# Optimization experiments

Hardware: AMD Instinct MI355X
Metric: run time of the kernel (lower is better)

## Reference

```python
import jax, jax.numpy as jnp
import numpy as np
import math

B, L, T, IN, H, DEPTH, HEADS = 4096, 1, 64, 16, 128, 3, 2
HD = H // HEADS
EPS = 1e-5


def layer_norm(x, g, b):
    u = jnp.mean(x, axis=-1, keepdims=True)
    s = jnp.mean((x - u) ** 2, axis=-1, keepdims=True)
    return g * (x - u) / jnp.sqrt(s + EPS) + b


def mlp(x, W, b, g, beta):
    return jax.nn.relu(layer_norm(x @ W + b, g, beta))


def attention(h, amask, Wq, bq, Wk, bk, Wv, bv):
    N, Tn, _ = h.shape
    def heads(x):
        return x.reshape(N, Tn, HEADS, HD).transpose(0, 2, 1, 3)
    q = heads(h @ Wq + bq)
    k = heads(h @ Wk + bk)
    v = heads(h @ Wv + bv)
    scores = jnp.einsum('nhqd,nhkd->nhqk', q, k) / math.sqrt(HD)
    scores = scores + (1.0 - amask[:, None]) * -10000.0
    probs = jax.nn.softmax(scores, axis=-1)
    ctx = jnp.einsum('nhqk,nhkd->nhqd', probs, v)
    return ctx.transpose(0, 2, 1, 3).reshape(N, Tn, H)


def setup_inputs() -> dict:
    key = jax.random.key(0)
    ks = jax.random.split(key, 8)
    feat = jax.random.normal(ks[0], (B, L, T, IN), jnp.float32)
    seq_lens = jax.random.randint(ks[1], (B, L), 1, T + 1)
    pos = jnp.arange(T)
    # repo convention: 0 = valid node, 1 = padded; prefix-valid layout
    masks = (pos[None, None, :] >= seq_lens[..., None]).astype(jnp.float32)[..., None]
    s = 0.02
    W_emb = jax.random.normal(ks[2], (IN, H), jnp.float32) * s
    W_enc = jax.random.normal(ks[3], (H, H), jnp.float32) * s
    Wq = jax.random.normal(ks[4], (DEPTH, H, H), jnp.float32) * s
    Wk = jax.random.normal(ks[5], (DEPTH, H, H), jnp.float32) * s
    Wv = jax.random.normal(ks[6], (DEPTH, H, H), jnp.float32) * s
    return dict(
        lane_nodes_feat=feat, masks=masks,
        W_emb=W_emb, b_emb=jnp.zeros((H,)), g_emb=jnp.ones((H,)), beta_emb=jnp.zeros((H,)),
        W_enc=W_enc, b_enc=jnp.zeros((H,)), g_enc=jnp.ones((H,)), beta_enc=jnp.zeros((H,)),
        Wq=Wq, bq=jnp.zeros((DEPTH, H)), Wk=Wk, bk=jnp.zeros((DEPTH, H)), Wv=Wv, bv=jnp.zeros((DEPTH, H)),
        ln_g=jnp.ones((DEPTH, H)), ln_b=jnp.zeros((DEPTH, H)),
    )


def reference(lane_nodes_feat, masks, W_emb, b_emb, g_emb, beta_emb, W_enc, b_enc,
              g_enc, beta_enc, Wq, bq, Wk, bk, Wv, bv, ln_g, ln_b):
    emb = mlp(lane_nodes_feat, W_emb, b_emb, g_emb, beta_emb)   # [B,L,T,H]
    emb = mlp(emb, W_enc, b_enc, g_enc, beta_enc)
    # every (b,l) lane has >=1 valid node by construction, so masked_select == reshape
    hs = emb.reshape(B * L, T, H)
    seq_lens = jnp.sum(1.0 - masks[:, :, :, 0], axis=-1).reshape(B * L)  # [N]
    pos = jnp.arange(T)
    valid = pos[None, :] < seq_lens[:, None]                              # [N,T]
    amask = (valid[:, :, None] & valid[:, None, :]).astype(hs.dtype)      # [N,T,T]
    for d in range(DEPTH):
        temp = hs
        hs = attention(hs, amask, Wq[d], bq[d], Wk[d], bk[d], Wv[d], bv[d])
        hs = jax.nn.relu(hs) + temp
        hs = layer_norm(hs, ln_g[d], ln_b[d])
    hs = jnp.max(hs, axis=1)                                              # [N,H]
    return hs.reshape(B, L, H)
```

## Files before the change

### kernel.cpp

```cpp
#include <hip/hip_runtime.h>

typedef unsigned short u16;
typedef unsigned int u32;
typedef __attribute__((ext_vector_type(8))) short short8;
typedef __attribute__((ext_vector_type(4))) float floatx4;

#define EPSV 1e-5f
#define WS_ELEMS 167936

__device__ __forceinline__ float b2f(u16 u){
  union { float f; u32 i; } c; c.i = ((u32)u) << 16; return c.f;
}
__device__ __forceinline__ u16 f2b(float f){
  union { float f; u32 i; } c; c.f = f;
  u32 r = c.i + 0x7FFFu + ((c.i >> 16) & 1u);
  return (u16)(r >> 16);
}
__device__ __forceinline__ u16 f2bc(float f){
  union { float f; u32 i; } c; c.f = f;
  return (u16)((c.i + 0x8000u) >> 16);
}
__device__ __forceinline__ float ldf(const void* p, int i, bool isf){
  return isf ? ((const float*)p)[i] : b2f(((const u16*)p)[i]);
}
__device__ __forceinline__ bool detect_f32(const void* g_emb){
  return *(const u32*)g_emb == 0x3F800000u;
}
__device__ __forceinline__ void dma16(const u16* g, u16* l){
  __builtin_amdgcn_global_load_lds((const __attribute__((address_space(1))) u32*)(g),
                                   (__attribute__((address_space(3))) u32*)(l), 16, 0, 0);
}
__device__ __forceinline__ void dma_slab(const u16* g, u16* dst, int wave, int lane){
  #pragma unroll
  for (int i = 0; i < 4; i++){
    int c = (wave << 2) + i;
    dma16(g + (c << 9) + (lane << 3), dst + (c << 9));
  }
}

__global__ void prep_kernel(const void* W_emb, const void* W_enc,
                            const void* Wq, const void* Wk, const void* Wv,
                            const void* g_emb, u16* ws){
  bool isf = detect_f32(g_emb);
  int e = blockIdx.x * 256 + threadIdx.x;
  if (e >= WS_ELEMS) return;
  float v;
  if (e < 4096){
    int half = e >> 11, r = e & 2047;
    int nt = r >> 9, q = (r >> 3) & 63, j = r & 7;
    int col = half*64 + nt*16 + (q & 15);
    int k = (q >> 4)*8 + j;
    v = (k < 16) ? ldf(W_emb, k*128 + col, isf) : 0.0f;
  } else if (e < 20480){
    int i = e - 4096;
    int half = i >> 13, r = i & 8191;
    int chunk = r >> 9, q = (r >> 3) & 63, j = r & 7;
    int ks = chunk >> 2, nt = chunk & 3;
    int col = half*64 + nt*16 + (q & 15);
    int k = ks*32 + (q >> 4)*8 + j;
    v = ldf(W_enc, k*128 + col, isf);
  } else {
    int i = e - 20480;
    int slab = i >> 13, r = i & 8191;
    int dh = slab / 3, which = slab - dh*3;
    int d = dh >> 1, h = dh & 1;
    int chunk = r >> 9, q = (r >> 3) & 63, j = r & 7;
    int ks = chunk >> 2, nt = chunk & 3;
    int col = h*64 + nt*16 + (q & 15);
    int k = ks*32 + (q >> 4)*8 + j;
    const void* W = (which == 0) ? Wv : (which == 1) ? Wk : Wq;
    v = ldf(W, d*16384 + k*128 + col, isf);
  }
  ws[e] = f2b(v);
}

__device__ __forceinline__ short8 frg(const u16* p, int chunk, int lane){
  return *(const short8*)(p + (chunk << 9) + (lane << 3));
}
__device__ __forceinline__ int wfoff(int wave, int nt, int lq, int lc){
  return ((((nt >> 1) << 2) + wave) << 9)
       + ((((((nt << 1) + (lc >> 3)) & 3) << 4) + (lq << 2)) << 3) + (lc & 7);
}
__device__ __forceinline__ int qfoff(int wave, int nt, int lq, int lc){
  return (wave << 10) + ((nt >> 1) << 9)
       + ((((((nt << 1) + (lc >> 3)) & 3) << 4) + (lq << 2)) << 3) + (lc & 7);
}

__device__ __forceinline__ void gemmW(const u16* sh, const u16* slab, int wave, int lane, floatx4* acc){
  #pragma unroll
  for (int ks = 0; ks < 4; ks++){
    short8 a = frg(sh, ks*4 + wave, lane);
    #pragma unroll
    for (int nt = 0; nt < 4; nt++)
      acc[nt] = __builtin_amdgcn_mfma_f32_16x16x32_bf16(a, frg(slab, ks*4 + nt, lane), acc[nt], 0, 0, 0);
  }
}
__device__ __forceinline__ void gemmWT(const u16* sh, const u16* slab, int wave, int lane, floatx4* acc){
  #pragma unroll
  for (int ks = 0; ks < 4; ks++){
    short8 a = frg(slab, ks*4 + wave, lane);
    #pragma unroll
    for (int nt = 0; nt < 4; nt++)
      acc[nt] = __builtin_amdgcn_mfma_f32_16x16x32_bf16(a, frg(sh, ks*4 + nt, lane), acc[nt], 0, 0, 0);
  }
}
__device__ __forceinline__ void gemm64(const u16* areg, const u16* b, int wave, int lane, floatx4* acc){
  #pragma unroll
  for (int ks = 0; ks < 2; ks++){
    short8 a = *(const short8*)(areg + (wave << 10) + (ks << 9) + (lane << 3));
    #pragma unroll
    for (int nt = 0; nt < 4; nt++)
      acc[nt] = __builtin_amdgcn_mfma_f32_16x16x32_bf16(a, frg(b, ks*4 + nt, lane), acc[nt], 0, 0, 0);
  }
}

__device__ __forceinline__ void red_sum2(float* s1, float* s2){
  #pragma unroll
  for (int m = 1; m < 16; m <<= 1){
    #pragma unroll
    for (int r = 0; r < 4; r++){
      s1[r] += __shfl_xor(s1[r], m, 64);
      s2[r] += __shfl_xor(s2[r], m, 64);
    }
  }
}

__device__ __forceinline__ void ln_mlp(floatx4* acc, const void* bias, const void* g,
    const void* bet, bool isf, float xres[8][4], int wave, int lq, int lc, u16* sh){
  float x[8][4], s1[4] = {0,0,0,0}, s2[4] = {0,0,0,0};
  #pragma unroll
  for (int nt = 0; nt < 8; nt++){
    float bb = ldf(bias, nt*16 + lc, isf);
    #pragma unroll
    for (int r = 0; r < 4; r++){
      float v = acc[nt][r] + bb;
      x[nt][r] = v; s1[r] += v; s2[r] += v*v;
    }
  }
  red_sum2(s1, s2);
  float mean[4], rstd[4];
  #pragma unroll
  for (int r = 0; r < 4; r++){
    mean[r] = s1[r] * (1.0f/128.0f);
    rstd[r] = rsqrtf(s2[r]*(1.0f/128.0f) - mean[r]*mean[r] + EPSV);
  }
  #pragma unroll
  for (int nt = 0; nt < 8; nt++){
    float gg = ldf(g, nt*16 + lc, isf), bb = ldf(bet, nt*16 + lc, isf);
    int o = wfoff(wave, nt, lq, lc);
    #pragma unroll
    for (int r = 0; r < 4; r++){
      float y = fmaxf((x[nt][r] - mean[r]) * rstd[r] * gg + bb, 0.0f);
      xres[nt][r] = y;
      sh[o + 8*r] = f2bc(y);
    }
  }
}

__device__ __forceinline__ void ln_attn(floatx4* ctx, float xres[8][4], const u16* cb,
                                        int wave, int lq, int lc, u16* sh){
  float x[8][4], s1[4] = {0,0,0,0}, s2[4] = {0,0,0,0};
  #pragma unroll
  for (int nt = 0; nt < 8; nt++){
    #pragma unroll
    for (int r = 0; r < 4; r++){
      float v = fmaxf(ctx[nt][r], 0.0f) + xres[nt][r];
      x[nt][r] = v; s1[r] += v; s2[r] += v*v;
    }
  }
  red_sum2(s1, s2);
  float mean[4], rstd[4];
  #pragma unroll
  for (int r = 0; r < 4; r++){
    mean[r] = s1[r] * (1.0f/128.0f);
    rstd[r] = rsqrtf(s2[r]*(1.0f/128.0f) - mean[r]*mean[r] + EPSV);
  }
  #pragma unroll
  for (int nt = 0; nt < 8; nt++){
    float gg = b2f(cb[384 + nt*16 + lc]), bb = b2f(cb[512 + nt*16 + lc]);
    int o = wfoff(wave, nt, lq, lc);
    #pragma unroll
    for (int r = 0; r < 4; r++){
      float y = (x[nt][r] - mean[r]) * rstd[r] * gg + bb;
      xres[nt][r] = y;
      sh[o + 8*r] = f2bc(y);
    }
  }
}

__global__ __launch_bounds__(256, 3)
void fused_kernel(const void* feat, const void* masks,
                  const void* b_emb, const void* g_emb, const void* be_emb,
                  const void* b_enc, const void* g_enc, const void* be_enc,
                  const void* bq, const void* bk, const void* bv,
                  const void* ln_g, const void* ln_b,
                  const u16* ws, void* out){
  __shared__ __align__(16) u16 s_h[8192];
  __shared__ __align__(16) u16 s_w[8192];
  __shared__ __align__(16) u16 s_k[4096];
  __shared__ __align__(16) u16 s_v[4096];
  __shared__ u16 s_c[1920];
  __shared__ float s_valid[64];

  int tid = threadIdx.x;
  int wave = tid >> 6, lane = tid & 63, lq = lane >> 4, lc = lane & 15;
  int n = blockIdx.x;
  bool isf = detect_f32(g_emb);
  const floatx4 z4 = {0.0f, 0.0f, 0.0f, 0.0f};

  dma16(ws + ((wave*2 + 0) << 9) + (lane << 3), s_w + ((wave*2 + 0) << 9));
  dma16(ws + ((wave*2 + 1) << 9) + (lane << 3), s_w + ((wave*2 + 1) << 9));

  if (!isf){
    const u16* fp = (const u16*)feat + n*1024;
    if (tid < 128){
      int t = tid >> 1, half = tid & 1;
      uint4 v = *(const uint4*)(fp + t*16 + half*8);
      *(uint4*)(s_h + ((t >> 4) << 9) + (((half << 4) + (t & 15)) << 3)) = v;
    } else {
      int t = (tid - 128) >> 1, half = 2 + ((tid - 128) & 1);
      uint4 z; z.x = 0; z.y = 0; z.z = 0; z.w = 0;
      *(uint4*)(s_h + ((t >> 4) << 9) + (((half << 4) + (t & 15)) << 3)) = z;
    }
  } else {
    for (int i = tid; i < 2048; i += 256){
      int t = i >> 5, k = i & 31;
      float v = (k < 16) ? ((const float*)feat)[n*1024 + t*16 + k] : 0.0f;
      s_h[((t >> 4) << 9) + ((((k >> 3) << 4) + (t & 15)) << 3) + (k & 7)] = f2b(v);
    }
  }
  for (int i = tid; i < 1920; i += 256){
    int blk = i >> 7, off = i & 127;
    int d = blk / 5, wh = blk - d*5;
    const void* src = (wh == 0) ? bq : (wh == 1) ? bk : (wh == 2) ? bv : (wh == 3) ? ln_g : ln_b;
    s_c[i] = isf ? f2b(((const float*)src)[d*128 + off]) : ((const u16*)src)[d*128 + off];
  }
  if (tid < 64) s_valid[tid] = (ldf(masks, n*64 + tid, isf) == 0.0f) ? 1.0f : 0.0f;
  __syncthreads();

  float xres[8][4];
  floatx4 acc[8];
  #pragma unroll
  for (int i = 0; i < 8; i++) acc[i] = z4;
  {
    short8 a = frg(s_h, wave, lane);
    #pragma unroll
    for (int nt = 0; nt < 4; nt++){
      acc[nt]     = __builtin_amdgcn_mfma_f32_16x16x32_bf16(a, frg(s_w, nt,     lane), acc[nt],     0,0,0);
      acc[4 + nt] = __builtin_amdgcn_mfma_f32_16x16x32_bf16(a, frg(s_w, 4 + nt, lane), acc[4 + nt], 0,0,0);
    }
  }
  __syncthreads();
  dma_slab(ws + 4096, s_w, wave, lane);
  ln_mlp(acc, b_emb, g_emb, be_emb, isf, xres, wave, lq, lc, s_h);
  __syncthreads();

  #pragma unroll
  for (int i = 0; i < 8; i++) acc[i] = z4;
  gemmW(s_h, s_w, wave, lane, acc);
  __syncthreads();
  dma_slab(ws + 12288, s_w, wave, lane);
  __syncthreads();
  gemmW(s_h, s_w, wave, lane, acc + 4);
  __syncthreads();
  dma_slab(ws + 20480, s_w, wave, lane);
  ln_mlp(acc, b_enc, g_enc, be_enc, isf, xres, wave, lq, lc, s_h);
  __syncthreads();

  int sb = 20480;
  for (int d = 0; d < 3; d++){
    const u16* cb = s_c + d*640;
    floatx4 ctx[8];
    #pragma unroll
    for (int i = 0; i < 8; i++) ctx[i] = z4;

    for (int h = 0; h < 2; h++){
      floatx4 pa[4];
      #pragma unroll
      for (int i = 0; i < 4; i++) pa[i] = z4;
      gemmWT(s_h, s_w, wave, lane, pa);
      __syncthreads();
      dma_slab(ws + sb + 8192, s_w, wave, lane);
      {
        float bb4[4];
        #pragma unroll
        for (int r = 0; r < 4; r++) bb4[r] = b2f(cb[256 + h*64 + wave*16 + (lq << 2) + r]);
        #pragma unroll
        for (int nt = 0; nt < 4; nt++){
          int o = wfoff(wave, nt, lq, lc);
          #pragma unroll
          for (int r = 0; r < 4; r++) s_v[o + 8*r] = f2bc(pa[nt][r] + bb4[r]);
        }
      }
      __syncthreads();
      #pragma unroll
      for (int i = 0; i < 4; i++) pa[i] = z4;
      gemmW(s_h, s_w, wave, lane, pa);
      __syncthreads();
      dma_slab(ws + sb + 16384, s_w, wave, lane);
      {
        #pragma unroll
        for (int nt = 0; nt < 4; nt++){
          float bb = b2f(cb[128 + h*64 + nt*16 + lc]);
          int o = wfoff(wave, nt, lq, lc);
          #pragma unroll
          for (int r = 0; r < 4; r++) s_k[o + 8*r] = f2bc(pa[nt][r] + bb);
        }
      }
      __syncthreads();
      #pragma unroll
      for (int i = 0; i < 4; i++) pa[i] = z4;
      gemmW(s_h, s_w, wave, lane, pa);
      __syncthreads();
      {
        #pragma unroll
        for (int nt = 0; nt < 4; nt++){
          float bb = b2f(cb[h*64 + nt*16 + lc]);
          int o = qfoff(wave, nt, lq, lc);
          #pragma unroll
          for (int r = 0; r < 4; r++) s_w[o + 8*r] = f2bc(pa[nt][r] + bb);
        }
      }
      #pragma unroll
      for (int i = 0; i < 4; i++) pa[i] = z4;
      gemm64(s_w, s_k, wave, lane, pa);

      float rv[4], cv[4];
      #pragma unroll
      for (int r = 0; r < 4; r++) rv[r] = s_valid[wave*16 + (lq << 2) + r];
      #pragma unroll
      for (int nt = 0; nt < 4; nt++) cv[nt] = s_valid[nt*16 + lc];

      float p[4][4];
      #pragma unroll
      for (int nt = 0; nt < 4; nt++)
        #pragma unroll
        for (int r = 0; r < 4; r++)
          p[nt][r] = pa[nt][r]*0.125f - 10000.0f*(1.0f - rv[r]*cv[nt]);

      float mx[4];
      #pragma unroll
      for (int r = 0; r < 4; r++)
        mx[r] = fmaxf(fmaxf(p[0][r], p[1][r]), fmaxf(p[2][r], p[3][r]));
      #pragma unroll
      for (int m = 1; m < 16; m <<= 1)
        #pragma unroll
        for (int r = 0; r < 4; r++) mx[r] = fmaxf(mx[r], __shfl_xor(mx[r], m, 64));

      float sm[4] = {0,0,0,0};
      #pragma unroll
      for (int nt = 0; nt < 4; nt++)
        #pragma unroll
        for (int r = 0; r < 4; r++){ p[nt][r] = __expf(p[nt][r] - mx[r]); sm[r] += p[nt][r]; }
      #pragma unroll
      for (int m = 1; m < 16; m <<= 1)
        #pragma unroll
        for (int r = 0; r < 4; r++) sm[r] += __shfl_xor(sm[r], m, 64);

      float inv[4];
      #pragma unroll
      for (int r = 0; r < 4; r++) inv[r] = 1.0f / sm[r];

      #pragma unroll
      for (int nt = 0; nt < 4; nt++){
        int o = qfoff(wave, nt, lq, lc);
        #pragma unroll
        for (int r = 0; r < 4; r++) s_w[o + 8*r] = f2bc(p[nt][r] * inv[r]);
      }
      gemm64(s_w, s_v, wave, lane, ctx + h*4);
      __syncthreads();
      sb += 24576;
      if (!(d == 2 && h == 1)) dma_slab(ws + sb, s_w, wave, lane);
      if (h == 1) ln_attn(ctx, xres, cb, wave, lq, lc, s_h);
      __syncthreads();
    }
  }

  if (tid < 128){
    int col = tid;
    float mxv = -1e30f;
    #pragma unroll 4
    for (int t = 0; t < 64; t++)
      mxv = fmaxf(mxv, b2f(s_h[((((col >> 5) << 2) + (t >> 4)) << 9)
                               + (((((col >> 3) & 3) << 4) + (t & 15)) << 3) + (col & 7)]));
    if (isf) ((float*)out)[n*128 + col] = mxv;
    else     ((u16*)out)[n*128 + col] = f2b(mxv);
  }
}

extern "C" void kernel_launch(void* const* d_in, const int* in_sizes, int n_in,
                              void* d_out, int out_size, void* d_ws, size_t ws_size,
                              hipStream_t stream){
  const void* feat   = d_in[0];
  const void* masks  = d_in[1];
  const void* W_emb  = d_in[2];
  const void* b_emb  = d_in[3];
  const void* g_emb  = d_in[4];
  const void* be_emb = d_in[5];
  const void* W_enc  = d_in[6];
  const void* b_enc  = d_in[7];
  const void* g_enc  = d_in[8];
  const void* be_enc = d_in[9];
  const void* Wq     = d_in[10];
  const void* bq     = d_in[11];
  const void* Wk     = d_in[12];
  const void* bk     = d_in[13];
  const void* Wv     = d_in[14];
  const void* bv     = d_in[15];
  const void* ln_g   = d_in[16];
  const void* ln_b   = d_in[17];
  u16* ws = (u16*)d_ws;

  hipLaunchKernelGGL(prep_kernel, dim3((WS_ELEMS + 255)/256), dim3(256), 0, stream,
                     W_emb, W_enc, Wq, Wk, Wv, g_emb, ws);
  hipLaunchKernelGGL(fused_kernel, dim3(4096), dim3(256), 0, stream,
                     feat, masks, b_emb, g_emb, be_emb, b_enc, g_enc, be_enc,
                     bq, bk, bv, ln_g, ln_b, ws, d_out);
}
```

Measured before the change: 383.1 us.

## Process two sequences per block to reuse weight slabs across both

Each block now handles two sequences, keeping two hidden-state tiles in shared memory and running every weight GEMM on both, so each staged weight slab (and its DMA and barriers) is amortised over twice the work. The grid is halved and launch bounds drop from 3 to 2 blocks per CU, because register use (two sets of accumulators and residuals) and LDS use both grow. The attention core is factored into a helper and run once per sequence, with the second sequence's Q/K/V results held in registers until the first finishes. The risk is lower occupancy and more register pressure, possibly spilling.

Measured after the change: 444.8 us. +16.1%, slower.

```diff
diff --git a/kernel.cpp b/kernel.cpp
--- a/kernel.cpp
+++ b/kernel.cpp
@@ -86,22 +86,32 @@
        + ((((((nt << 1) + (lc >> 3)) & 3) << 4) + (lq << 2)) << 3) + (lc & 7);
 }
 
-__device__ __forceinline__ void gemmW(const u16* sh, const u16* slab, int wave, int lane, floatx4* acc){
+#define MFMA(a,b,c) __builtin_amdgcn_mfma_f32_16x16x32_bf16((a),(b),(c),0,0,0)
+
+__device__ __forceinline__ void gemmW2(const u16* sh0, const u16* sh1, const u16* slab,
+                                       int wave, int lane, floatx4* a0v, floatx4* a1v){
   #pragma unroll
   for (int ks = 0; ks < 4; ks++){
-    short8 a = frg(sh, ks*4 + wave, lane);
-    #pragma unroll
-    for (int nt = 0; nt < 4; nt++)
-      acc[nt] = __builtin_amdgcn_mfma_f32_16x16x32_bf16(a, frg(slab, ks*4 + nt, lane), acc[nt], 0, 0, 0);
-  }
-}
-__device__ __forceinline__ void gemmWT(const u16* sh, const u16* slab, int wave, int lane, floatx4* acc){
+    short8 a0 = frg(sh0, ks*4 + wave, lane);
+    short8 a1 = frg(sh1, ks*4 + wave, lane);
+    #pragma unroll
+    for (int nt = 0; nt < 4; nt++){
+      short8 b = frg(slab, ks*4 + nt, lane);
+      a0v[nt] = MFMA(a0, b, a0v[nt]);
+      a1v[nt] = MFMA(a1, b, a1v[nt]);
+    }
+  }
+}
+__device__ __forceinline__ void gemmWT2(const u16* sh0, const u16* sh1, const u16* slab,
+                                        int wave, int lane, floatx4* a0v, floatx4* a1v){
   #pragma unroll
   for (int ks = 0; ks < 4; ks++){
     short8 a = frg(slab, ks*4 + wave, lane);
     #pragma unroll
-    for (int nt = 0; nt < 4; nt++)
-      acc[nt] = __builtin_amdgcn_mfma_f32_16x16x32_bf16(a, frg(sh, ks*4 + nt, lane), acc[nt], 0, 0, 0);
+    for (int nt = 0; nt < 4; nt++){
+      a0v[nt] = MFMA(a, frg(sh0, ks*4 + nt, lane), a0v[nt]);
+      a1v[nt] = MFMA(a, frg(sh1, ks*4 + nt, lane), a1v[nt]);
+    }
   }
 }
 __device__ __forceinline__ void gemm64(const u16* areg, const u16* b, int wave, int lane, floatx4* acc){
@@ -110,7 +120,7 @@
     short8 a = *(const short8*)(areg + (wave << 10) + (ks << 9) + (lane << 3));
     #pragma unroll
     for (int nt = 0; nt < 4; nt++)
-      acc[nt] = __builtin_amdgcn_mfma_f32_16x16x32_bf16(a, frg(b, ks*4 + nt, lane), acc[nt], 0, 0, 0);
+      acc[nt] = MFMA(a, frg(b, ks*4 + nt, lane), acc[nt]);
   }
 }
 
@@ -188,23 +198,98 @@
   }
 }
 
-__global__ __launch_bounds__(256, 3)
+__device__ __forceinline__ void put_col(floatx4* pa, const u16* bias, u16* dst, bool qreg,
+                                        int wave, int lq, int lc){
+  #pragma unroll
+  for (int nt = 0; nt < 4; nt++){
+    float bb = b2f(bias[nt*16 + lc]);
+    int o = qreg ? qfoff(wave, nt, lq, lc) : wfoff(wave, nt, lq, lc);
+    #pragma unroll
+    for (int r = 0; r < 4; r++) dst[o + 8*r] = f2bc(pa[nt][r] + bb);
+  }
+}
+__device__ __forceinline__ void put_v(floatx4* pa, const float* bb4, u16* dst,
+                                      int wave, int lq, int lc){
+  #pragma unroll
+  for (int nt = 0; nt < 4; nt++){
+    int o = wfoff(wave, nt, lq, lc);
+    #pragma unroll
+    for (int r = 0; r < 4; r++) dst[o + 8*r] = f2bc(pa[nt][r] + bb4[r]);
+  }
+}
+
+__device__ __forceinline__ void attn_core(const float* sval, u16* s_w, const u16* s_k,
+                                          const u16* s_v, int wave, int lane, int lq, int lc,
+                                          floatx4* ctx4){
+  const floatx4 z4 = {0.0f, 0.0f, 0.0f, 0.0f};
+  floatx4 pa[4];
+  #pragma unroll
+  for (int i = 0; i < 4; i++) pa[i] = z4;
+  gemm64(s_w, s_k, wave, lane, pa);
+
+  float rv[4], cv[4];
+  #pragma unroll
+  for (int r = 0; r < 4; r++) rv[r] = sval[wave*16 + (lq << 2) + r];
+  #pragma unroll
+  for (int nt = 0; nt < 4; nt++) cv[nt] = sval[nt*16 + lc];
+
+  float p[4][4];
+  #pragma unroll
+  for (int nt = 0; nt < 4; nt++)
+    #pragma unroll
+    for (int r = 0; r < 4; r++)
+      p[nt][r] = pa[nt][r]*0.125f - 10000.0f*(1.0f - rv[r]*cv[nt]);
+
+  float mx[4];
+  #pragma unroll
+  for (int r = 0; r < 4; r++)
+    mx[r] = fmaxf(fmaxf(p[0][r], p[1][r]), fmaxf(p[2][r], p[3][r]));
+  #pragma unroll
+  for (int m = 1; m < 16; m <<= 1)
+    #pragma unroll
+    for (int r = 0; r < 4; r++) mx[r] = fmaxf(mx[r], __shfl_xor(mx[r], m, 64));
+
+  float sm[4] = {0,0,0,0};
+  #pragma unroll
+  for (int nt = 0; nt < 4; nt++)
+    #pragma unroll
+    for (int r = 0; r < 4; r++){ p[nt][r] = __expf(p[nt][r] - mx[r]); sm[r] += p[nt][r]; }
+  #pragma unroll
+  for (int m = 1; m < 16; m <<= 1)
+    #pragma unroll
+    for (int r = 0; r < 4; r++) sm[r] += __shfl_xor(sm[r], m, 64);
+
+  float inv[4];
+  #pragma unroll
+  for (int r = 0; r < 4; r++) inv[r] = 1.0f / sm[r];
+
+  #pragma unroll
+  for (int nt = 0; nt < 4; nt++){
+    int o = qfoff(wave, nt, lq, lc);
+    #pragma unroll
+    for (int r = 0; r < 4; r++) s_w[o + 8*r] = f2bc(p[nt][r] * inv[r]);
+  }
+  gemm64(s_w, s_v, wave, lane, ctx4);
+}
+
+__global__ __launch_bounds__(256, 2)
 void fused_kernel(const void* feat, const void* masks,
                   const void* b_emb, const void* g_emb, const void* be_emb,
                   const void* b_enc, const void* g_enc, const void* be_enc,
                   const void* bq, const void* bk, const void* bv,
                   const void* ln_g, const void* ln_b,
                   const u16* ws, void* out){
-  __shared__ __align__(16) u16 s_h[8192];
+  __shared__ __align__(16) u16 s_h0[8192];
+  __shared__ __align__(16) u16 s_h1[8192];
   __shared__ __align__(16) u16 s_w[8192];
   __shared__ __align__(16) u16 s_k[4096];
   __shared__ __align__(16) u16 s_v[4096];
   __shared__ u16 s_c[1920];
-  __shared__ float s_valid[64];
+  __shared__ float s_valid[128];
 
   int tid = threadIdx.x;
   int wave = tid >> 6, lane = tid & 63, lq = lane >> 4, lc = lane & 15;
-  int n = blockIdx.x;
+  int n0 = blockIdx.x * 2;
   bool isf = detect_f32(g_emb);
   const floatx4 z4 = {0.0f, 0.0f, 0.0f, 0.0f};
 
@@ -212,21 +297,28 @@
   dma16(ws + ((wave*2 + 1) << 9) + (lane << 3), s_w + ((wave*2 + 1) << 9));
 
   if (!isf){
-    const u16* fp = (const u16*)feat + n*1024;
-    if (tid < 128){
-      int t = tid >> 1, half = tid & 1;
-      uint4 v = *(const uint4*)(fp + t*16 + half*8);
-      *(uint4*)(s_h + ((t >> 4) << 9) + (((half << 4) + (t & 15)) << 3)) = v;
-    } else {
-      int t = (tid - 128) >> 1, half = 2 + ((tid - 128) & 1);
-      uint4 z; z.x = 0; z.y = 0; z.z = 0; z.w = 0;
-      *(uint4*)(s_h + ((t >> 4) << 9) + (((half << 4) + (t & 15)) << 3)) = z;
+    const u16* fp = (const u16*)feat + (size_t)n0*1024;
+    #pragma unroll
+    for (int rep = 0; rep < 2; rep++){
+      int i = rep*256 + tid;
+      int seq = i >> 8, j = i & 255;
+      u16* sh = seq ? s_h1 : s_h0;
+      if (j < 128){
+        int t = j >> 1, half = j & 1;
+        uint4 v = *(const uint4*)(fp + seq*1024 + t*16 + half*8);
+        *(uint4*)(sh + ((t >> 4) << 9) + (((half << 4) + (t & 15)) << 3)) = v;
+      } else {
+        int t = (j - 128) >> 1, half = 2 + ((j - 128) & 1);
+        uint4 z; z.x = 0; z.y = 0; z.z = 0; z.w = 0;
+        *(uint4*)(sh + ((t >> 4) << 9) + (((half << 4) + (t & 15)) << 3)) = z;
+      }
     }
   } else {
-    for (int i = tid; i < 2048; i += 256){
-      int t = i >> 5, k = i & 31;
-      float v = (k < 16) ? ((const float*)feat)[n*1024 + t*16 + k] : 0.0f;
-      s_h[((t >> 4) << 9) + ((((k >> 3) << 4) + (t & 15)) << 3) + (k & 7)] = f2b(v);
+    for (int i = tid; i < 4096; i += 256){
+      int seq = i >> 11, j = i & 2047;
+      int t = j >> 5, k = j & 31;
+      float v = (k < 16) ? ((const float*)feat)[(size_t)(n0 + seq)*1024 + t*16 + k] : 0.0f;
+      (seq ? s_h1 : s_h0)[((t >> 4) << 9) + ((((k >> 3) << 4) + (t & 15)) << 3) + (k & 7)] = f2b(v);
     }
   }
   for (int i = tid; i < 1920; i += 256){
@@ -235,156 +327,102 @@
     const void* src = (wh == 0) ? bq : (wh == 1) ? bk : (wh == 2) ? bv : (wh == 3) ? ln_g : ln_b;
     s_c[i] = isf ? f2b(((const float*)src)[d*128 + off]) : ((const u16*)src)[d*128 + off];
   }
-  if (tid < 64) s_valid[tid] = (ldf(masks, n*64 + tid, isf) == 0.0f) ? 1.0f : 0.0f;
-  __syncthreads();
-
-  float xres[8][4];
-  floatx4 acc[8];
-  #pragma unroll
-  for (int i = 0; i < 8; i++) acc[i] = z4;
+  if (tid < 128) s_valid[tid] = (ldf(masks, n0*64 + tid, isf) == 0.0f) ? 1.0f : 0.0f;
+  __syncthreads();
+
+  float xres0[8][4], xres1[8][4];
+  floatx4 acc0[8], acc1[8];
+  #pragma unroll
+  for (int i = 0; i < 8; i++){ acc0[i] = z4; acc1[i] = z4; }
   {
-    short8 a = frg(s_h, wave, lane);
+    short8 a0 = frg(s_h0, wave, lane);
+    short8 a1 = frg(s_h1, wave, lane);
     #pragma unroll
     for (int nt = 0; nt < 4; nt++){
-      acc[nt]     = __builtin_amdgcn_mfma_f32_16x16x32_bf16(a, frg(s_w, nt,     lane), acc[nt],     0,0,0);
-      acc[4 + nt] = __builtin_amdgcn_mfma_f32_16x16x32_bf16(a, frg(s_w, 4 + nt, lane), acc[4 + nt], 0,0,0);
+      short8 b = frg(s_w, nt, lane);
+      acc0[nt] = MFMA(a0, b, acc0[nt]);  acc1[nt] = MFMA(a1, b, acc1[nt]);
+      short8 b2 = frg(s_w, 4 + nt, lane);
+      acc0[4+nt] = MFMA(a0, b2, acc0[4+nt]);  acc1[4+nt] = MFMA(a1, b2, acc1[4+nt]);
     }
   }
   __syncthreads();
   dma_slab(ws + 4096, s_w, wave, lane);
-  ln_mlp(acc, b_emb, g_emb, be_emb, isf, xres, wave, lq, lc, s_h);
-  __syncthreads();
-
-  #pragma unroll
-  for (int i = 0; i < 8; i++) acc[i] = z4;
-  gemmW(s_h, s_w, wave, lane, acc);
+  ln_mlp(acc0, b_emb, g_emb, be_emb, isf, xres0, wave, lq, lc, s_h0);
+  ln_mlp(acc1, b_emb, g_emb, be_emb, isf, xres1, wave, lq, lc, s_h1);
+  __syncthreads();
+
+  #pragma unroll
+  for (int i = 0; i < 8; i++){ acc0[i] = z4; acc1[i] = z4; }
+  gemmW2(s_h0, s_h1, s_w, wave, lane, acc0, acc1);
   __syncthreads();
   dma_slab(ws + 12288, s_w, wave, lane);
   __syncthreads();
-  gemmW(s_h, s_w, wave, lane, acc + 4);
+  gemmW2(s_h0, s_h1, s_w, wave, lane, acc0 + 4, acc1 + 4);
   __syncthreads();
   dma_slab(ws + 20480, s_w, wave, lane);
-  ln_mlp(acc, b_enc, g_enc, be_enc, isf, xres, wave, lq, lc, s_h);
+  ln_mlp(acc0, b_enc, g_enc, be_enc, isf, xres0, wave, lq, lc, s_h0);
+  ln_mlp(acc1, b_enc, g_enc, be_enc, isf, xres1, wave, lq, lc, s_h1);
   __syncthreads();
 
   int sb = 20480;
   for (int d = 0; d < 3; d++){
     const u16* cb = s_c + d*640;
-    floatx4 ctx[8];
-    #pragma unroll
-    for (int i = 0; i < 8; i++) ctx[i] = z4;
+    floatx4 ctx0[8], ctx1[8];
+    #pragma unroll
+    for (int i = 0; i < 8; i++){ ctx0[i] = z4; ctx1[i] = z4; }
 
     for (int h = 0; h < 2; h++){
-      floatx4 pa[4];
+      floatx4 pv0[4], pv1[4], pk0[4], pk1[4], pq0[4], pq1[4];
       #pragma unroll
-      for (int i = 0; i < 4; i++) pa[i] = z4;
-      gemmWT(s_h, s_w, wave, lane, pa);
+      for (int i = 0; i < 4; i++){ pv0[i] = z4; pv1[i] = z4; }
+      gemmWT2(s_h0, s_h1, s_w, wave, lane, pv0, pv1);
       __syncthreads();
       dma_slab(ws + sb + 8192, s_w, wave, lane);
-      {
-        float bb4[4];
-        #pragma unroll
-        for (int r = 0; r < 4; r++) bb4[r] = b2f(cb[256 + h*64 + wave*16 + (lq << 2) + r]);
-        #pragma unroll
-        for (int nt = 0; nt < 4; nt++){
-          int o = wfoff(wave, nt, lq, lc);
-          #pragma unroll
-          for (int r = 0; r < 4; r++) s_v[o + 8*r] = f2bc(pa[nt][r] + bb4[r]);
-        }
-      }
-      __syncthreads();
+      float bb4[4];
       #pragma unroll
-      for (int i = 0; i < 4; i++) pa[i] = z4;
-      gemmW(s_h, s_w, wave, lane, pa);
+      for (int r = 0; r < 4; r++) bb4[r] = b2f(cb[256 + h*64 + wave*16 + (lq << 2) + r]);
+      put_v(pv0, bb4, s_v, wave, lq, lc);
+      __syncthreads();
+      #pragma unroll
+      for (int i = 0; i < 4; i++){ pk0[i] = z4; pk1[i] = z4; }
+      gemmW2(s_h0, s_h1, s_w, wave, lane, pk0, pk1);
       __syncthreads();
       dma_slab(ws + sb + 16384, s_w, wave, lane);
-      {
-        #pragma unroll
-        for (int nt = 0; nt < 4; nt++){
-          float bb = b2f(cb[128 + h*64 + nt*16 + lc]);
-          int o = wfoff(wave, nt, lq, lc);
-          #pragma unroll
-          for (int r = 0; r < 4; r++) s_k[o + 8*r] = f2bc(pa[nt][r] + bb);
-        }
-      }
+      put_col(pk0, cb + 128 + h*64, s_k, false, wave, lq, lc);
       __syncthreads();
       #pragma unroll
-      for (int i = 0; i < 4; i++) pa[i] = z4;
-      gemmW(s_h, s_w, wave, lane, pa);
-      __syncthreads();
-      {
-        #pragma unroll
-        for (int nt = 0; nt < 4; nt++){
-          float bb = b2f(cb[h*64 + nt*16 + lc]);
-          int o = qfoff(wave, nt, lq, lc);
-          #pragma unroll
-          for (int r = 0; r < 4; r++) s_w[o + 8*r] = f2bc(pa[nt][r] + bb);
-        }
-      }
-      #pragma unroll
-      for (int i = 0; i < 4; i++) pa[i] = z4;
-      gemm64(s_w, s_k, wave, lane, pa);
-
-      float rv[4], cv[4];
-      #pragma unroll
-      for (int r = 0; r < 4; r++) rv[r] = s_valid[wave*16 + (lq << 2) + r];
-      #pragma unroll
-      for (int nt = 0; nt < 4; nt++) cv[nt] = s_valid[nt*16 + lc];
-
-      float p[4][4];
-      #pragma unroll
-      for (int nt = 0; nt < 4; nt++)
-        #pragma unroll
-        for (int r = 0; r < 4; r++)
-          p[nt][r] = pa[nt][r]*0.125f - 10000.0f*(1.0f - rv[r]*cv[nt]);
-
-      float mx[4];
-      #pragma unroll
-      for (int r = 0; r < 4; r++)
-        mx[r] = fmaxf(fmaxf(p[0][r], p[1][r]), fmaxf(p[2][r], p[3][r]));
-      #pragma unroll
-      for (int m = 1; m < 16; m <<= 1)
-        #pragma unroll
-        for (int r = 0; r < 4; r++) mx[r] = fmaxf(mx[r], __shfl_xor(mx[r], m, 64));
-
-      float sm[4] = {0,0,0,0};
-      #pragma unroll
-      for (int nt = 0; nt < 4; nt++)
-        #pragma unroll
-        for (int r = 0; r < 4; r++){ p[nt][r] = __expf(p[nt][r] - mx[r]); sm[r] += p[nt][r]; }
-      #pragma unroll
-      for (int m = 1; m < 16; m <<= 1)
-        #pragma unroll
-        for (int r = 0; r < 4; r++) sm[r] += __shfl_xor(sm[r], m, 64);
-
-      float inv[4];
-      #pragma unroll
-      for (int r = 0; r < 4; r++) inv[r] = 1.0f / sm[r];
-
-      #pragma unroll
-      for (int nt = 0; nt < 4; nt++){
-        int o = qfoff(wave, nt, lq, lc);
-        #pragma unroll
-        for (int r = 0; r < 4; r++) s_w[o + 8*r] = f2bc(p[nt][r] * inv[r]);
-      }
-      gemm64(s_w, s_v, wave, lane, ctx + h*4);
+      for (int i = 0; i < 4; i++){ pq0[i] = z4; pq1[i] = z4; }
+      gemmW2(s_h0, s_h1, s_w, wave, lane, pq0, pq1);
+      __syncthreads();
+      put_col(pq0, cb + h*64, s_w, true, wave, lq, lc);
+      attn_core(s_valid, s_w, s_k, s_v, wave, lane, lq, lc, ctx0 + h*4);
+      __syncthreads();
+      put_v(pv1, bb4, s_v, wave, lq, lc);
+      put_col(pk1, cb + 128 + h*64, s_k, false, wave, lq, lc);
+      put_col(pq1, cb + h*64, s_w, true, wave, lq, lc);
+      __syncthreads();
+      attn_core(s_valid + 64, s_w, s_k, s_v, wave, lane, lq, lc, ctx1 + h*4);
       __syncthreads();
       sb += 24576;
       if (!(d == 2 && h == 1)) dma_slab(ws + sb, s_w, wave, lane);
-      if (h == 1) ln_attn(ctx, xres, cb, wave, lq, lc, s_h);
-      __syncthreads();
-    }
-  }
-
-  if (tid < 128){
-    int col = tid;
+      if (h == 1){
+        ln_attn(ctx0, xres0, cb, wave, lq, lc, s_h0);
+        ln_attn(ctx1, xres1, cb, wave, lq, lc, s_h1);
+      }
+      __syncthreads();
+    }
+  }
+
+  {
+    int seq = tid >> 7, col = tid & 127;
+    const u16* shp = seq ? s_h1 : s_h0;
     float mxv = -1e30f;
     #pragma unroll 4
     for (int t = 0; t < 64; t++)
-      mxv = fmaxf(mxv, b2f(s_h[((((col >> 5) << 2) + (t >> 4)) << 9)
+      mxv = fmaxf(mxv, b2f(shp[((((col >> 5) << 2) + (t >> 4)) << 9)
                                + (((((col >> 3) & 3) << 4) + (t & 15)) << 3) + (col & 7)]));
-    if (isf) ((float*)out)[n*128 + col] = mxv;
-    else     ((u16*)out)[n*128 + col] = f2b(mxv);
+    if (isf) ((float*)out)[(size_t)(n0 + seq)*128 + col] = mxv;
+    else     ((u16*)out)[(size_t)(n0 + seq)*128 + col] = f2b(mxv);
   }
 }
 
@@ -413,7 +451,7 @@
 
   hipLaunchKernelGGL(prep_kernel, dim3((WS_ELEMS + 255)/256), dim3(256), 0, stream,
                      W_emb, W_enc, Wq, Wk, Wv, g_emb, ws);
-  hipLaunchKernelGGL(fused_kernel, dim3(4096), dim3(256), 0, stream,
+  hipLaunchKernelGGL(fused_kernel, dim3(2048), dim3(256), 0, stream,
                      feat, masks, b_emb, g_emb, be_emb, b_enc, g_enc, be_enc,
                      bq, bk, bv, ln_g, ln_b, ws, d_out);
 }
```

## Cut LDS footprint and registers to raise occupancy to four blocks per CU

Applied to the files above, without the earlier changes.

Removes the shared-memory copies of biases, LayerNorm params and the valid mask, which are now read from global memory or held in registers. K is staged inside the upper half of s_w and V alone in s_kv, so the block's LDS drops to about 40 KB. The kernel now asks for four blocks per CU instead of three. The 1/sqrt(HD) scale is folded into Q before the bf16 store, and the temporary x arrays in the LayerNorm helpers are replaced by xres to save registers. The cost is an extra barrier, repeated global bias loads, and possible spills under the tighter register limit.

New measurement: 407.3 us. +6.3%, slower.

```diff
diff --git a/kernel.cpp b/kernel.cpp
--- a/kernel.cpp
+++ b/kernel.cpp
@@ -86,13 +86,15 @@
        + ((((((nt << 1) + (lc >> 3)) & 3) << 4) + (lq << 2)) << 3) + (lc & 7);
 }
 
+#define MFMA(a,b,c) __builtin_amdgcn_mfma_f32_16x16x32_bf16((a),(b),(c),0,0,0)
+
 __device__ __forceinline__ void gemmW(const u16* sh, const u16* slab, int wave, int lane, floatx4* acc){
   #pragma unroll
   for (int ks = 0; ks < 4; ks++){
     short8 a = frg(sh, ks*4 + wave, lane);
     #pragma unroll
     for (int nt = 0; nt < 4; nt++)
-      acc[nt] = __builtin_amdgcn_mfma_f32_16x16x32_bf16(a, frg(slab, ks*4 + nt, lane), acc[nt], 0, 0, 0);
+      acc[nt] = MFMA(a, frg(slab, ks*4 + nt, lane), acc[nt]);
   }
 }
 __device__ __forceinline__ void gemmWT(const u16* sh, const u16* slab, int wave, int lane, floatx4* acc){
@@ -101,7 +103,7 @@
     short8 a = frg(slab, ks*4 + wave, lane);
     #pragma unroll
     for (int nt = 0; nt < 4; nt++)
-      acc[nt] = __builtin_amdgcn_mfma_f32_16x16x32_bf16(a, frg(sh, ks*4 + nt, lane), acc[nt], 0, 0, 0);
+      acc[nt] = MFMA(a, frg(sh, ks*4 + nt, lane), acc[nt]);
   }
 }
 __device__ __forceinline__ void gemm64(const u16* areg, const u16* b, int wave, int lane, floatx4* acc){
@@ -110,7 +112,7 @@
     short8 a = *(const short8*)(areg + (wave << 10) + (ks << 9) + (lane << 3));
     #pragma unroll
     for (int nt = 0; nt < 4; nt++)
-      acc[nt] = __builtin_amdgcn_mfma_f32_16x16x32_bf16(a, frg(b, ks*4 + nt, lane), acc[nt], 0, 0, 0);
+      acc[nt] = MFMA(a, frg(b, ks*4 + nt, lane), acc[nt]);
   }
 }
 
@@ -127,14 +129,14 @@
 
 __device__ __forceinline__ void ln_mlp(floatx4* acc, const void* bias, const void* g,
     const void* bet, bool isf, float xres[8][4], int wave, int lq, int lc, u16* sh){
-  float x[8][4], s1[4] = {0,0,0,0}, s2[4] = {0,0,0,0};
+  float s1[4] = {0,0,0,0}, s2[4] = {0,0,0,0};
   #pragma unroll
   for (int nt = 0; nt < 8; nt++){
     float bb = ldf(bias, nt*16 + lc, isf);
     #pragma unroll
     for (int r = 0; r < 4; r++){
       float v = acc[nt][r] + bb;
-      x[nt][r] = v; s1[r] += v; s2[r] += v*v;
+      xres[nt][r] = v; s1[r] += v; s2[r] += v*v;
     }
   }
   red_sum2(s1, s2);
@@ -150,22 +152,23 @@
     int o = wfoff(wave, nt, lq, lc);
     #pragma unroll
     for (int r = 0; r < 4; r++){
-      float y = fmaxf((x[nt][r] - mean[r]) * rstd[r] * gg + bb, 0.0f);
+      float y = fmaxf((xres[nt][r] - mean[r]) * rstd[r] * gg + bb, 0.0f);
       xres[nt][r] = y;
       sh[o + 8*r] = f2bc(y);
     }
   }
 }
 
-__device__ __forceinline__ void ln_attn(floatx4* ctx, float xres[8][4], const u16* cb,
-                                        int wave, int lq, int lc, u16* sh){
-  float x[8][4], s1[4] = {0,0,0,0}, s2[4] = {0,0,0,0};
+__device__ __forceinline__ void ln_attn(floatx4* ctx, float xres[8][4],
+    const void* g, const void* bet, int goff, bool isf,
+    int wave, int lq, int lc, u16* sh){
+  float s1[4] = {0,0,0,0}, s2[4] = {0,0,0,0};
   #pragma unroll
   for (int nt = 0; nt < 8; nt++){
     #pragma unroll
     for (int r = 0; r < 4; r++){
       float v = fmaxf(ctx[nt][r], 0.0f) + xres[nt][r];
-      x[nt][r] = v; s1[r] += v; s2[r] += v*v;
+      xres[nt][r] = v; s1[r] += v; s2[r] += v*v;
     }
   }
   red_sum2(s1, s2);
@@ -177,18 +180,18 @@
   }
   #pragma unroll
   for (int nt = 0; nt < 8; nt++){
-    float gg = b2f(cb[384 + nt*16 + lc]), bb = b2f(cb[512 + nt*16 + lc]);
+    float gg = ldf(g, goff + nt*16 + lc, isf), bb = ldf(bet, goff + nt*16 + lc, isf);
     int o = wfoff(wave, nt, lq, lc);
     #pragma unroll
     for (int r = 0; r < 4; r++){
-      float y = (x[nt][r] - mean[r]) * rstd[r] * gg + bb;
+      float y = (xres[nt][r] - mean[r]) * rstd[r] * gg + bb;
       xres[nt][r] = y;
       sh[o + 8*r] = f2bc(y);
     }
   }
 }
 
-__global__ __launch_bounds__(256, 3)
+__global__ __launch_bounds__(256, 4)
 void fused_kernel(const void* feat, const void* masks,
                   const void* b_emb, const void* g_emb, const void* be_emb,
                   const void* b_enc, const void* g_enc, const void* be_enc,
@@ -197,10 +200,7 @@
                   const u16* ws, void* out){
   __shared__ __align__(16) u16 s_h[8192];
   __shared__ __align__(16) u16 s_w[8192];
-  __shared__ __align__(16) u16 s_k[4096];
-  __shared__ __align__(16) u16 s_v[4096];
-  __shared__ u16 s_c[1920];
-  __shared__ float s_valid[64];
+  __shared__ __align__(16) u16 s_kv[4096];
 
   int tid = threadIdx.x;
   int wave = tid >> 6, lane = tid & 63, lq = lane >> 4, lc = lane & 15;
@@ -212,7 +212,7 @@
   dma16(ws + ((wave*2 + 1) << 9) + (lane << 3), s_w + ((wave*2 + 1) << 9));
 
   if (!isf){
-    const u16* fp = (const u16*)feat + n*1024;
+    const u16* fp = (const u16*)feat + (size_t)n*1024;
     if (tid < 128){
       int t = tid >> 1, half = tid & 1;
       uint4 v = *(const uint4*)(fp + t*16 + half*8);
@@ -225,17 +225,17 @@
   } else {
     for (int i = tid; i < 2048; i += 256){
       int t = i >> 5, k = i & 31;
-      float v = (k < 16) ? ((const float*)feat)[n*1024 + t*16 + k] : 0.0f;
+      float v = (k < 16) ? ((const float*)feat)[(size_t)n*1024 + t*16 + k] : 0.0f;
       s_h[((t >> 4) << 9) + ((((k >> 3) << 4) + (t & 15)) << 3) + (k & 7)] = f2b(v);
     }
   }
-  for (int i = tid; i < 1920; i += 256){
-    int blk = i >> 7, off = i & 127;
-    int d = blk / 5, wh = blk - d*5;
-    const void* src = (wh == 0) ? bq : (wh == 1) ? bk : (wh == 2) ? bv : (wh == 3) ? ln_g : ln_b;
-    s_c[i] = isf ? f2b(((const float*)src)[d*128 + off]) : ((const u16*)src)[d*128 + off];
-  }
-  if (tid < 64) s_valid[tid] = (ldf(masks, n*64 + tid, isf) == 0.0f) ? 1.0f : 0.0f;
+  float rv[4], cv[4];
+  #pragma unroll
+  for (int r = 0; r < 4; r++)
+    rv[r] = (ldf(masks, n*64 + wave*16 + lq*4 + r, isf) == 0.0f) ? 1.0f : 0.0f;
+  #pragma unroll
+  for (int nt = 0; nt < 4; nt++)
+    cv[nt] = (ldf(masks, n*64 + nt*16 + lc, isf) == 0.0f) ? 1.0f : 0.0f;
   __syncthreads();
 
   float xres[8][4];
@@ -246,8 +246,8 @@
     short8 a = frg(s_h, wave, lane);
     #pragma unroll
     for (int nt = 0; nt < 4; nt++){
-      acc[nt]     = __builtin_amdgcn_mfma_f32_16x16x32_bf16(a, frg(s_w, nt,     lane), acc[nt],     0,0,0);
-      acc[4 + nt] = __builtin_amdgcn_mfma_f32_16x16x32_bf16(a, frg(s_w, 4 + nt, lane), acc[4 + nt], 0,0,0);
+      acc[nt]     = MFMA(a, frg(s_w, nt,     lane), acc[nt]);
+      acc[4 + nt] = MFMA(a, frg(s_w, 4 + nt, lane), acc[4 + nt]);
     }
   }
   __syncthreads();
@@ -269,74 +269,66 @@
 
   int sb = 20480;
   for (int d = 0; d < 3; d++){
-    const u16* cb = s_c + d*640;
     floatx4 ctx[8];
     #pragma unroll
     for (int i = 0; i < 8; i++) ctx[i] = z4;
 
     for (int h = 0; h < 2; h++){
-      floatx4 pa[4];
-      #pragma unroll
-      for (int i = 0; i < 4; i++) pa[i] = z4;
-      gemmWT(s_h, s_w, wave, lane, pa);
+      int cbase = d*128 + h*64;
+      floatx4 pv[4], pk[4], pq[4];
+      #pragma unroll
+      for (int i = 0; i < 4; i++) pv[i] = z4;
+      gemmWT(s_h, s_w, wave, lane, pv);
       __syncthreads();
       dma_slab(ws + sb + 8192, s_w, wave, lane);
       {
         float bb4[4];
         #pragma unroll
-        for (int r = 0; r < 4; r++) bb4[r] = b2f(cb[256 + h*64 + wave*16 + (lq << 2) + r]);
+        for (int r = 0; r < 4; r++) bb4[r] = ldf(bv, cbase + wave*16 + (lq << 2) + r, isf);
         #pragma unroll
         for (int nt = 0; nt < 4; nt++){
           int o = wfoff(wave, nt, lq, lc);
           #pragma unroll
-          for (int r = 0; r < 4; r++) s_v[o + 8*r] = f2bc(pa[nt][r] + bb4[r]);
+          for (int r = 0; r < 4; r++) s_kv[o + 8*r] = f2bc(pv[nt][r] + bb4[r]);
         }
       }
       __syncthreads();
       #pragma unroll
+      for (int i = 0; i < 4; i++) pk[i] = z4;
+      gemmW(s_h, s_w, wave, lane, pk);
+      __syncthreads();
+      dma_slab(ws + sb + 16384, s_w, wave, lane);
+      __syncthreads();
+      #pragma unroll
+      for (int i = 0; i < 4; i++) pq[i] = z4;
+      gemmW(s_h, s_w, wave, lane, pq);
+      __syncthreads();
+      #pragma unroll
+      for (int nt = 0; nt < 4; nt++){
+        float bb = ldf(bk, cbase + nt*16 + lc, isf);
+        int o = wfoff(wave, nt, lq, lc);
+        #pragma unroll
+        for (int r = 0; r < 4; r++) s_w[4096 + o + 8*r] = f2bc(pk[nt][r] + bb);
+      }
+      #pragma unroll
+      for (int nt = 0; nt < 4; nt++){
+        float bb = ldf(bq, cbase + nt*16 + lc, isf);
+        int o = qfoff(wave, nt, lq, lc);
+        #pragma unroll
+        for (int r = 0; r < 4; r++) s_w[o + 8*r] = f2bc((pq[nt][r] + bb) * 0.125f);
+      }
+      __syncthreads();
+      floatx4 pa[4];
+      #pragma unroll
       for (int i = 0; i < 4; i++) pa[i] = z4;
-      gemmW(s_h, s_w, wave, lane, pa);
-      __syncthreads();
-      dma_slab(ws + sb + 16384, s_w, wave, lane);
-      {
-        #pragma unroll
-        for (int nt = 0; nt < 4; nt++){
-          float bb = b2f(cb[128 + h*64 + nt*16 + lc]);
-          int o = wfoff(wave, nt, lq, lc);
-          #pragma unroll
-          for (int r = 0; r < 4; r++) s_k[o + 8*r] = f2bc(pa[nt][r] + bb);
-        }
-      }
-      __syncthreads();
-      #pragma unroll
-      for (int i = 0; i < 4; i++) pa[i] = z4;
-      gemmW(s_h, s_w, wave, lane, pa);
-      __syncthreads();
-      {
-        #pragma unroll
-        for (int nt = 0; nt < 4; nt++){
-          float bb = b2f(cb[h*64 + nt*16 + lc]);
-          int o = qfoff(wave, nt, lq, lc);
-          #pragma unroll
-          for (int r = 0; r < 4; r++) s_w[o + 8*r] = f2bc(pa[nt][r] + bb);
-        }
-      }
-      #pragma unroll
-      for (int i = 0; i < 4; i++) pa[i] = z4;
-      gemm64(s_w, s_k, wave, lane, pa);
-
-      float rv[4], cv[4];
-      #pragma unroll
-      for (int r = 0; r < 4; r++) rv[r] = s_valid[wave*16 + (lq << 2) + r];
-      #pragma unroll
-      for (int nt = 0; nt < 4; nt++) cv[nt] = s_valid[nt*16 + lc];
+      gemm64(s_w, s_w + 4096, wave, lane, pa);
 
       float p[4][4];
       #pragma unroll
       for (int nt = 0; nt < 4; nt++)
         #pragma unroll
         for (int r = 0; r < 4; r++)
-          p[nt][r] = pa[nt][r]*0.125f - 10000.0f*(1.0f - rv[r]*cv[nt]);
+          p[nt][r] = pa[nt][r] - 10000.0f*(1.0f - rv[r]*cv[nt]);
 
       float mx[4];
       #pragma unroll
@@ -367,11 +359,11 @@
         #pragma unroll
         for (int r = 0; r < 4; r++) s_w[o + 8*r] = f2bc(p[nt][r] * inv[r]);
       }
-      gemm64(s_w, s_v, wave, lane, ctx + h*4);
+      gemm64(s_w, s_kv, wave, lane, ctx + h*4);
       __syncthreads();
       sb += 24576;
       if (!(d == 2 && h == 1)) dma_slab(ws + sb, s_w, wave, lane);
-      if (h == 1) ln_attn(ctx, xres, cb, wave, lq, lc, s_h);
+      if (h == 1) ln_attn(ctx, xres, ln_g, ln_b, d*128, isf, wave, lq, lc, s_h);
       __syncthreads();
     }
   }
@@ -383,8 +375,8 @@
     for (int t = 0; t < 64; t++)
       mxv = fmaxf(mxv, b2f(s_h[((((col >> 5) << 2) + (t >> 4)) << 9)
                                + (((((col >> 3) & 3) << 4) + (t & 15)) << 3) + (col & 7)]));
-    if (isf) ((float*)out)[n*128 + col] = mxv;
-    else     ((u16*)out)[n*128 + col] = f2b(mxv);
+    if (isf) ((float*)out)[(size_t)n*128 + col] = mxv;
+    else     ((u16*)out)[(size_t)n*128 + col] = f2b(mxv);
   }
 }
 
```
